# Performance work log

Measured on AMD Instinct MI355X. Metric: run time of the kernel, lower is better.

## Reference

```python
import jax, jax.numpy as jnp
import numpy as np

ALPHA = 0.2  # LeakyReLU negative slope
NEG_INF = -1e9


def setup_inputs() -> dict:
    key = jax.random.key(0)
    k1, k2, k3, k4 = jax.random.split(key, 4)
    B, N, Fin, Fout = 8, 2048, 128, 64
    h = jax.random.normal(k1, (B, N, Fin), dtype=jnp.float32)
    adj_mask = jax.random.randint(k2, (B, N, N), 0, 2).astype(jnp.int32)
    # xavier_uniform-style scales
    W = jax.random.uniform(k3, (Fout, Fin), dtype=jnp.float32,
                           minval=-1.0, maxval=1.0) * np.sqrt(6.0 / (Fin + Fout))
    a = jax.random.uniform(k4, (2 * Fout,), dtype=jnp.float32,
                           minval=-1.0, maxval=1.0) * np.sqrt(6.0 / (2 * Fout + 1))
    return {"h": h, "adj_mask": adj_mask, "W": W, "a": a}


def reference(h, adj_mask, W, a):
    # Wh: [B, N, Fout]
    Wh = jnp.einsum("bnf,of->bno", h, W)
    Fout = Wh.shape[-1]
    a1, a2 = a[:Fout], a[Fout:]
    # additive decomposition of a([Wh_i || Wh_j]): e_ij = leakyrelu(s1_i + s2_j)
    s1 = Wh @ a1  # [B, N]
    s2 = Wh @ a2  # [B, N]
    e = jax.nn.leaky_relu(s1[:, :, None] + s2[:, None, :], negative_slope=ALPHA)  # [B,N,N]
    e = jnp.where(adj_mask == 0, NEG_INF, e)
    attention = jax.nn.softmax(e, axis=-1)
    # dropout is identity in eval mode / p effectively 0 for the reference
    h_prime = jnp.einsum("bij,bjo->bio", attention, Wh)
    return h_prime
```

## Files before the change

kernel.cpp:

```cpp
#include <hip/hip_runtime.h>
#include <hip/hip_fp16.h>
#include <math.h>

#define LRELU_ALPHA 0.2f
#define NEG_INF -1000000000.0f
#define L2E 1.44269504088896340736f

constexpr int B_ = 8, N_ = 2048, FIN = 128, FOUT = 64;

typedef _Float16 __attribute__((ext_vector_type(8))) f16x8;
typedef float __attribute__((ext_vector_type(4))) f32x4;

__device__ __forceinline__ void gload16(const void* g, void* l) {
  __builtin_amdgcn_global_load_lds(
      (const __attribute__((address_space(1))) void*)g,
      (__attribute__((address_space(3))) void*)l, 16, 0, 0);
}

__global__ __launch_bounds__(256) void k_wh(
    const float* __restrict__ h, const float* __restrict__ W,
    const float* __restrict__ a, unsigned short* __restrict__ WhT,
    float* __restrict__ s1, float* __restrict__ s2) {
  __shared__ float Wt[128][65];
  __shared__ float hs[16][128];

  const int t = threadIdx.x;
  const int row0 = blockIdx.x * 16;

  for (int e = t; e < 64 * 128; e += 256) {
    int o = e >> 7, f = e & 127;
    Wt[f][o] = W[e];
  }
  {
    const float4* hg = (const float4*)(h + (size_t)row0 * FIN);
    for (int i4 = t; i4 < 16 * 32; i4 += 256) {
      int r = i4 >> 5, f4 = i4 & 31;
      *(float4*)&hs[r][f4 * 4] = hg[i4];
    }
  }
  __syncthreads();

  const int wave = t >> 6, lane = t & 63;
  float acc[4] = {0.f, 0.f, 0.f, 0.f};
#pragma unroll 4
  for (int f4 = 0; f4 < 32; ++f4) {
    float w0 = Wt[4 * f4 + 0][lane], w1 = Wt[4 * f4 + 1][lane];
    float w2 = Wt[4 * f4 + 2][lane], w3 = Wt[4 * f4 + 3][lane];
#pragma unroll
    for (int r = 0; r < 4; ++r) {
      float4 hv = *(const float4*)&hs[wave * 4 + r][f4 * 4];
      acc[r] += hv.x * w0 + hv.y * w1 + hv.z * w2 + hv.w * w3;
    }
  }

  const float a1v = a[lane], a2v = a[64 + lane];
  const int b = row0 / N_;
#pragma unroll
  for (int r = 0; r < 4; ++r) {
    const int row = row0 + wave * 4 + r;
    const int n = row - b * N_;
    const float v = acc[r];
    WhT[((size_t)b * 64 + lane) * N_ + n] = __half_as_ushort(__float2half(v));
    float p1 = v * a1v, p2 = v * a2v;
#pragma unroll
    for (int d = 32; d; d >>= 1) {
      p1 += __shfl_xor(p1, d, 64);
      p2 += __shfl_xor(p2, d, 64);
    }
    if (lane == 0) { s1[row] = p1; s2[row] = p2; }
  }
}

__global__ __launch_bounds__(256, 2) void k_attn(
    const unsigned short* __restrict__ WhT,
    const float* __restrict__ s1g, const float* __restrict__ s2g,
    const int* __restrict__ adj, float* __restrict__ out) {
  __shared__ __align__(16) unsigned char sbuf[4][8 * 1024];
  __shared__ float s2s[N_];

  const int t = threadIdx.x;
  const int wave = t >> 6, lane = t & 63;
  const int m = lane & 15, q = lane >> 4;
  const int b = blockIdx.y;
  const int i0 = blockIdx.x * 32;
  const int rg = wave & 1;
  const int p0 = (wave >> 1) * 2;

  const unsigned short* whB = WhT + (size_t)b * 64 * N_;
  const int* adjR = adj + (size_t)b * N_ * N_ + (size_t)(i0 + rg * 16 + m) * N_;

  {
    const float4* s2R = (const float4*)(s2g + (size_t)b * N_);
    for (int i = t; i < N_ / 4; i += 256) {
      float4 v = s2R[i];
      v.x *= L2E; v.y *= L2E; v.z *= L2E; v.w *= L2E;
      ((float4*)s2s)[i] = v;
    }
  }

  const float s1r = s1g[b * N_ + i0 + rg * 16 + m];
  const float c1 = (s1r - 2.0f) * L2E;
  const float c2 = (LRELU_ALPHA * s1r - 2.0f) * L2E;

  f16x8 ones;
#pragma unroll
  for (int j = 0; j < 8; ++j) ones[j] = (_Float16)1.0f;

  const unsigned char* whP0 =
      (const unsigned char*)(whB + (size_t)(wave * 16 + m) * N_ + q * 8);
  const unsigned char* whP1 = whP0 + 64;

#define STAGE(c)                                                            \
  {                                                                         \
    gload16(whP0 + (size_t)(c) * 128, &sbuf[(c) & 3][(wave * 2 + 0) * 1024]); \
    gload16(whP1 + (size_t)(c) * 128, &sbuf[(c) & 3][(wave * 2 + 1) * 1024]); \
  }
#define ISSUE_ADJ(S, c)                 \
  {                                     \
    const int* ap = adjR + (c) * 64 + q * 8; \
    S##0 = *(const int4*)(ap);          \
    S##1 = *(const int4*)(ap + 4);      \
    S##2 = *(const int4*)(ap + 32);     \
    S##3 = *(const int4*)(ap + 36);     \
  }
#define CONSUME(S, c)                                                        \
  {                                                                          \
    const unsigned char* Bb = &sbuf[(c) & 3][0];                             \
    _Pragma("unroll") for (int ks = 0; ks < 2; ++ks) {                       \
      int4 A0 = ks ? S##2 : S##0;                                            \
      int4 A1 = ks ? S##3 : S##1;                                            \
      const float* sp = &s2s[(c) * 64 + ks * 32 + q * 8];                    \
      float4 sv0 = *(const float4*)sp;                                       \
      float4 sv1 = *(const float4*)(sp + 4);                                 \
      float xs[8] = {sv0.x, sv0.y, sv0.z, sv0.w, sv1.x, sv1.y, sv1.z, sv1.w};\
      int avs[8] = {A0.x, A0.y, A0.z, A0.w, A1.x, A1.y, A1.z, A1.w};         \
      f16x8 af;                                                              \
      _Pragma("unroll") for (int j = 0; j < 8; ++j) {                        \
        float x = xs[j];                                                     \
        float e = fmaxf(c1 + x, fmaf(LRELU_ALPHA, x, c2));                   \
        e = avs[j] ? e : NEG_INF;                                            \
        af[j] = (_Float16)__builtin_amdgcn_exp2f(e);        \
      }                                                                      \
      f16x8 b0 = *(const f16x8*)(Bb + ((p0 + 0) * 2 + ks) * 1024 + lane * 16);\
      f16x8 b1 = *(const f16x8*)(Bb + ((p0 + 1) * 2 + ks) * 1024 + lane * 16);\
      acc0 = __builtin_amdgcn_mfma_f32_16x16x32_f16(af, b0, acc0, 0, 0, 0);  \
      acc1 = __builtin_amdgcn_mfma_f32_16x16x32_f16(af, b1, acc1, 0, 0, 0);  \
      accS = __builtin_amdgcn_mfma_f32_16x16x32_f16(af, ones, accS, 0, 0, 0);\
    }                                                                        \
  }
#define ITERX(c, S, VMS)                        \
  {                                             \
    asm volatile("s_waitcnt " VMS ::: "memory");\
    __builtin_amdgcn_s_barrier();               \
    CONSUME(S, c)                               \
  }

  int4 rA0, rA1, rA2, rA3, rB0, rB1, rB2, rB3, rC0, rC1, rC2, rC3;
  f32x4 acc0 = {0.f, 0.f, 0.f, 0.f}, acc1 = acc0, accS = acc0;

  ISSUE_ADJ(rA, 0) STAGE(0)
  ISSUE_ADJ(rB, 1) STAGE(1)
  ISSUE_ADJ(rC, 2) STAGE(2)
  __syncthreads();

  for (int cb = 0; cb < 27; cb += 3) {
    ITERX(cb + 0, rA, "vmcnt(12)") ISSUE_ADJ(rA, cb + 3) STAGE(cb + 3)
    ITERX(cb + 1, rB, "vmcnt(12)") ISSUE_ADJ(rB, cb + 4) STAGE(cb + 4)
    ITERX(cb + 2, rC, "vmcnt(12)") ISSUE_ADJ(rC, cb + 5) STAGE(cb + 5)
  }
  ITERX(27, rA, "vmcnt(12)") ISSUE_ADJ(rA, 30) STAGE(30)
  ITERX(28, rB, "vmcnt(12)") ISSUE_ADJ(rB, 31) STAGE(31)
  ITERX(29, rC, "vmcnt(12)")
  ITERX(30, rA, "vmcnt(6)")
  ITERX(31, rB, "vmcnt(0)")

#pragma unroll
  for (int r = 0; r < 4; ++r) {
    const int ri = q * 4 + r;
    const float l = accS[r];
    const float inv = (l == 0.f) ? 1.f : 1.f / l;
    const size_t row = (size_t)b * N_ + i0 + rg * 16 + ri;
    out[row * FOUT + (p0 + 0) * 16 + m] = acc0[r] * inv;
    out[row * FOUT + (p0 + 1) * 16 + m] = acc1[r] * inv;
  }
#undef STAGE
#undef ISSUE_ADJ
#undef CONSUME
#undef ITERX
}

extern "C" void kernel_launch(void* const* d_in, const int* in_sizes, int n_in,
                              void* d_out, int out_size, void* d_ws, size_t ws_size,
                              hipStream_t stream) {
  const float* h   = (const float*)d_in[0];
  const int*   adj = (const int*)d_in[1];
  const float* W   = (const float*)d_in[2];
  const float* a   = (const float*)d_in[3];
  float* out = (float*)d_out;

  unsigned short* WhT = (unsigned short*)d_ws;
  float* s1 = (float*)(WhT + (size_t)B_ * 64 * N_);
  float* s2 = s1 + (size_t)B_ * N_;

  k_wh<<<dim3(B_ * N_ / 16), 256, 0, stream>>>(h, W, a, WhT, s1, s2);
  k_attn<<<dim3(N_ / 32, B_), 256, 0, stream>>>(WhT, s1, s2, adj, out);
}
```

Before: 226.6 us.

## Bit-pack adjacency mask, split attention over key halves, add reduction kernel

A new pre-pass kernel reads the int32 adjacency mask once and packs it into 64-bit ballot words, laid out so each lane can pull its 8 mask bits per step. The attention kernel then reads the packed mask instead of int4 loads of int32 values. It loads WhT straight into registers rather than staging it through LDS with barriers, and splits the key dimension into two halves across a third grid axis, with a higher occupancy launch bound. Partial outputs and row sums go to workspace, and a small normalisation kernel combines them. This trades an extra full pass over the mask plus a partial-result round trip for a leaner, better-occupied main loop.

```diff
diff --git a/kernel.cpp b/kernel.cpp
--- a/kernel.cpp
+++ b/kernel.cpp
@@ -10,12 +10,6 @@
 
 typedef _Float16 __attribute__((ext_vector_type(8))) f16x8;
 typedef float __attribute__((ext_vector_type(4))) f32x4;
-
-__device__ __forceinline__ void gload16(const void* g, void* l) {
-  __builtin_amdgcn_global_load_lds(
-      (const __attribute__((address_space(1))) void*)g,
-      (__attribute__((address_space(3))) void*)l, 16, 0, 0);
-}
 
 __global__ __launch_bounds__(256) void k_wh(
     const float* __restrict__ h, const float* __restrict__ W,
@@ -71,122 +65,146 @@
   }
 }
 
-__global__ __launch_bounds__(256, 2) void k_attn(
+__global__ __launch_bounds__(256) void k_pack(
+    const int* __restrict__ adj, unsigned long long* __restrict__ pk) {
+  const int wave = threadIdx.x >> 6, lane = threadIdx.x & 63;
+  const size_t wid = (size_t)blockIdx.x * 4 + wave;
+  const int* src = adj + wid * 64 * 64 + lane;
+  unsigned long long* dst = pk + wid * 64;
+  for (int it = 0; it < 64; ++it) {
+    int v = src[it * 64];
+    unsigned long long mask = __ballot(v != 0);
+    unsigned long long o = 0;
+#pragma unroll
+    for (int qq = 0; qq < 4; ++qq) {
+      unsigned long long b0 = (mask >> (8 * qq)) & 0xFFull;
+      unsigned long long b1 = (mask >> (32 + 8 * qq)) & 0xFFull;
+      o |= (b0 | (b1 << 8)) << (16 * qq);
+    }
+    if (lane == 0) dst[it] = o;
+  }
+}
+
+__global__ __launch_bounds__(256, 4) void k_attn(
     const unsigned short* __restrict__ WhT,
     const float* __restrict__ s1g, const float* __restrict__ s2g,
-    const int* __restrict__ adj, float* __restrict__ out) {
-  __shared__ __align__(16) unsigned char sbuf[4][8 * 1024];
-  __shared__ float s2s[N_];
+    const unsigned short* __restrict__ pk,
+    float* __restrict__ pAcc, float* __restrict__ pSum) {
+  __shared__ float s2s[N_ / 2];
 
   const int t = threadIdx.x;
   const int wave = t >> 6, lane = t & 63;
   const int m = lane & 15, q = lane >> 4;
   const int b = blockIdx.y;
   const int i0 = blockIdx.x * 32;
+  const int js = blockIdx.z;
+  const int j0 = js * (N_ / 2);
   const int rg = wave & 1;
   const int p0 = (wave >> 1) * 2;
 
-  const unsigned short* whB = WhT + (size_t)b * 64 * N_;
-  const int* adjR = adj + (size_t)b * N_ * N_ + (size_t)(i0 + rg * 16 + m) * N_;
-
   {
-    const float4* s2R = (const float4*)(s2g + (size_t)b * N_);
-    for (int i = t; i < N_ / 4; i += 256) {
-      float4 v = s2R[i];
-      v.x *= L2E; v.y *= L2E; v.z *= L2E; v.w *= L2E;
-      ((float4*)s2s)[i] = v;
-    }
-  }
-
-  const float s1r = s1g[b * N_ + i0 + rg * 16 + m];
+    const float4* s2R = (const float4*)(s2g + (size_t)b * N_ + j0);
+    float4 v = s2R[t];
+    v.x *= L2E; v.y *= L2E; v.z *= L2E; v.w *= L2E;
+    ((float4*)s2s)[t] = v;
+  }
+
+  const int row_i = i0 + rg * 16 + m;
+  const float s1r = s1g[b * N_ + row_i];
   const float c1 = (s1r - 2.0f) * L2E;
   const float c2 = (LRELU_ALPHA * s1r - 2.0f) * L2E;
 
+  const unsigned short* whB = WhT + (size_t)b * 64 * N_;
+  const unsigned short* bp0 = whB + (size_t)(p0 * 16 + m) * N_ + j0 + q * 8;
+  const unsigned short* bp1 = whB + (size_t)((p0 + 1) * 16 + m) * N_ + j0 + q * 8;
+  const unsigned short* pkL =
+      pk + ((size_t)(b * N_ + row_i) * 32 + js * 16) * 4 + q;
+
   f16x8 ones;
 #pragma unroll
   for (int j = 0; j < 8; ++j) ones[j] = (_Float16)1.0f;
 
-  const unsigned char* whP0 =
-      (const unsigned char*)(whB + (size_t)(wave * 16 + m) * N_ + q * 8);
-  const unsigned char* whP1 = whP0 + 64;
-
-#define STAGE(c)                                                            \
-  {                                                                         \
-    gload16(whP0 + (size_t)(c) * 128, &sbuf[(c) & 3][(wave * 2 + 0) * 1024]); \
-    gload16(whP1 + (size_t)(c) * 128, &sbuf[(c) & 3][(wave * 2 + 1) * 1024]); \
-  }
-#define ISSUE_ADJ(S, c)                 \
-  {                                     \
-    const int* ap = adjR + (c) * 64 + q * 8; \
-    S##0 = *(const int4*)(ap);          \
-    S##1 = *(const int4*)(ap + 4);      \
-    S##2 = *(const int4*)(ap + 32);     \
-    S##3 = *(const int4*)(ap + 36);     \
-  }
-#define CONSUME(S, c)                                                        \
+  __syncthreads();
+
+  f32x4 acc0 = {0.f, 0.f, 0.f, 0.f}, acc1 = acc0, accS = acc0;
+
+  unsigned sA_w, sB_w;
+  f16x8 sA_b00, sA_b01, sA_b10, sA_b11;
+  f16x8 sB_b00, sB_b01, sB_b10, sB_b11;
+
+#define ISSUE(P, c)                                  \
+  {                                                  \
+    P##_w = (unsigned)pkL[(c) * 4];                  \
+    P##_b00 = *(const f16x8*)(bp0 + (c) * 64);       \
+    P##_b01 = *(const f16x8*)(bp0 + (c) * 64 + 32);  \
+    P##_b10 = *(const f16x8*)(bp1 + (c) * 64);       \
+    P##_b11 = *(const f16x8*)(bp1 + (c) * 64 + 32);  \
+  }
+#define CONSUME(P, c)                                                        \
   {                                                                          \
-    const unsigned char* Bb = &sbuf[(c) & 3][0];                             \
     _Pragma("unroll") for (int ks = 0; ks < 2; ++ks) {                       \
-      int4 A0 = ks ? S##2 : S##0;                                            \
-      int4 A1 = ks ? S##3 : S##1;                                            \
       const float* sp = &s2s[(c) * 64 + ks * 32 + q * 8];                    \
       float4 sv0 = *(const float4*)sp;                                       \
       float4 sv1 = *(const float4*)(sp + 4);                                 \
       float xs[8] = {sv0.x, sv0.y, sv0.z, sv0.w, sv1.x, sv1.y, sv1.z, sv1.w};\
-      int avs[8] = {A0.x, A0.y, A0.z, A0.w, A1.x, A1.y, A1.z, A1.w};         \
+      unsigned wb = P##_w >> (ks * 8);                                       \
       f16x8 af;                                                              \
       _Pragma("unroll") for (int j = 0; j < 8; ++j) {                        \
         float x = xs[j];                                                     \
         float e = fmaxf(c1 + x, fmaf(LRELU_ALPHA, x, c2));                   \
-        e = avs[j] ? e : NEG_INF;                                            \
+        e = ((wb >> j) & 1u) ? e : NEG_INF;                                  \
         af[j] = (_Float16)__builtin_amdgcn_exp2f(e);        \
       }                                                                      \
-      f16x8 b0 = *(const f16x8*)(Bb + ((p0 + 0) * 2 + ks) * 1024 + lane * 16);\
-      f16x8 b1 = *(const f16x8*)(Bb + ((p0 + 1) * 2 + ks) * 1024 + lane * 16);\
-      acc0 = __builtin_amdgcn_mfma_f32_16x16x32_f16(af, b0, acc0, 0, 0, 0);  \
-      acc1 = __builtin_amdgcn_mfma_f32_16x16x32_f16(af, b1, acc1, 0, 0, 0);  \
+      f16x8 B0 = ks ? P##_b01 : P##_b00;                                     \
+      f16x8 B1 = ks ? P##_b11 : P##_b10;                                     \
+      acc0 = __builtin_amdgcn_mfma_f32_16x16x32_f16(af, B0, acc0, 0, 0, 0);  \
+      acc1 = __builtin_amdgcn_mfma_f32_16x16x32_f16(af, B1, acc1, 0, 0, 0);  \
       accS = __builtin_amdgcn_mfma_f32_16x16x32_f16(af, ones, accS, 0, 0, 0);\
     }                                                                        \
   }
-#define ITERX(c, S, VMS)                        \
-  {                                             \
-    asm volatile("s_waitcnt " VMS ::: "memory");\
-    __builtin_amdgcn_s_barrier();               \
-    CONSUME(S, c)                               \
-  }
-
-  int4 rA0, rA1, rA2, rA3, rB0, rB1, rB2, rB3, rC0, rC1, rC2, rC3;
-  f32x4 acc0 = {0.f, 0.f, 0.f, 0.f}, acc1 = acc0, accS = acc0;
-
-  ISSUE_ADJ(rA, 0) STAGE(0)
-  ISSUE_ADJ(rB, 1) STAGE(1)
-  ISSUE_ADJ(rC, 2) STAGE(2)
-  __syncthreads();
-
-  for (int cb = 0; cb < 27; cb += 3) {
-    ITERX(cb + 0, rA, "vmcnt(12)") ISSUE_ADJ(rA, cb + 3) STAGE(cb + 3)
-    ITERX(cb + 1, rB, "vmcnt(12)") ISSUE_ADJ(rB, cb + 4) STAGE(cb + 4)
-    ITERX(cb + 2, rC, "vmcnt(12)") ISSUE_ADJ(rC, cb + 5) STAGE(cb + 5)
-  }
-  ITERX(27, rA, "vmcnt(12)") ISSUE_ADJ(rA, 30) STAGE(30)
-  ITERX(28, rB, "vmcnt(12)") ISSUE_ADJ(rB, 31) STAGE(31)
-  ITERX(29, rC, "vmcnt(12)")
-  ITERX(30, rA, "vmcnt(6)")
-  ITERX(31, rB, "vmcnt(0)")
+#define FENCE(VMS) asm volatile("s_waitcnt " VMS ::: "memory");
+
+  ISSUE(sA, 0)
+  ISSUE(sB, 1)
+  for (int c = 0; c < 14; c += 2) {
+    FENCE("vmcnt(5)")
+    CONSUME(sA, c) ISSUE(sA, c + 2)
+    FENCE("vmcnt(5)")
+    CONSUME(sB, c + 1) ISSUE(sB, c + 3)
+  }
+  FENCE("vmcnt(5)")
+  CONSUME(sA, 14)
+  FENCE("vmcnt(0)")
+  CONSUME(sB, 15)
 
 #pragma unroll
   for (int r = 0; r < 4; ++r) {
     const int ri = q * 4 + r;
-    const float l = accS[r];
-    const float inv = (l == 0.f) ? 1.f : 1.f / l;
-    const size_t row = (size_t)b * N_ + i0 + rg * 16 + ri;
-    out[row * FOUT + (p0 + 0) * 16 + m] = acc0[r] * inv;
-    out[row * FOUT + (p0 + 1) * 16 + m] = acc1[r] * inv;
-  }
-#undef STAGE
-#undef ISSUE_ADJ
+    const size_t row = (size_t)js * B_ * N_ + (size_t)b * N_ + i0 + rg * 16 + ri;
+    pAcc[row * FOUT + (p0 + 0) * 16 + m] = acc0[r];
+    pAcc[row * FOUT + (p0 + 1) * 16 + m] = acc1[r];
+    if (p0 == 0 && m == 0) pSum[row] = accS[r];
+  }
+#undef ISSUE
 #undef CONSUME
-#undef ITERX
+#undef FENCE
+}
+
+__global__ __launch_bounds__(256) void k_norm(
+    const float* __restrict__ pAcc, const float* __restrict__ pSum,
+    float* __restrict__ out) {
+  const int i4 = blockIdx.x * 256 + threadIdx.x;
+  const int row = i4 >> 4;
+  float4 v0 = ((const float4*)pAcc)[i4];
+  float4 v1 = ((const float4*)pAcc)[i4 + B_ * N_ * FOUT / 4];
+  const float l = pSum[row] + pSum[B_ * N_ + row];
+  const float inv = (l == 0.f) ? 1.f : 1.f / l;
+  float4 o;
+  o.x = (v0.x + v1.x) * inv;
+  o.y = (v0.y + v1.y) * inv;
+  o.z = (v0.z + v1.z) * inv;
+  o.w = (v0.w + v1.w) * inv;
+  ((float4*)out)[i4] = o;
 }
 
 extern "C" void kernel_launch(void* const* d_in, const int* in_sizes, int n_in,
@@ -201,7 +219,13 @@
   unsigned short* WhT = (unsigned short*)d_ws;
   float* s1 = (float*)(WhT + (size_t)B_ * 64 * N_);
   float* s2 = s1 + (size_t)B_ * N_;
-
+  float* pAcc = s2 + (size_t)B_ * N_;
+  float* pSum = pAcc + (size_t)2 * B_ * N_ * FOUT;
+  unsigned long long* pkw = (unsigned long long*)(pSum + (size_t)2 * B_ * N_);
+
+  k_pack<<<dim3(2048), 256, 0, stream>>>(adj, pkw);
   k_wh<<<dim3(B_ * N_ / 16), 256, 0, stream>>>(h, W, a, WhT, s1, s2);
-  k_attn<<<dim3(N_ / 32, B_), 256, 0, stream>>>(WhT, s1, s2, adj, out);
-}
+  k_attn<<<dim3(N_ / 32, B_, 2), 256, 0, stream>>>(
+      WhT, s1, s2, (const unsigned short*)pkw, pAcc, pSum);
+  k_norm<<<dim3(B_ * N_ * FOUT / 1024), 256, 0, stream>>>(pAcc, pSum, out);
+}
```

Result: slower. 272.3 us (+20.2%).

## Pre-pack adjacency mask into LDS bitmasks via ballot before attention loop

Applied to the files above, without the earlier changes.

The kernel no longer streams int32 adjacency values through registers inside the pipelined loop. Each block now reads its 32 rows of the mask up front with coalesced int4 loads, packs them into 64-bit ballot bitmasks in shared memory, and the main loop pulls mask bits from LDS. The loop becomes a 4-stage ring that only prefetches Wh tiles, with fewer outstanding vector loads and registers. The trade-off is a serialized prologue that reads all 256 KB of the block's mask before any compute can overlap it, plus extra bit-extraction ALU work in the inner loop.

```diff
diff --git a/kernel.cpp b/kernel.cpp
--- a/kernel.cpp
+++ b/kernel.cpp
@@ -76,6 +76,7 @@
     const float* __restrict__ s1g, const float* __restrict__ s2g,
     const int* __restrict__ adj, float* __restrict__ out) {
   __shared__ __align__(16) unsigned char sbuf[4][8 * 1024];
+  __shared__ unsigned long long pkls[32][34];
   __shared__ float s2s[N_];
 
   const int t = threadIdx.x;
@@ -86,8 +87,8 @@
   const int rg = wave & 1;
   const int p0 = (wave >> 1) * 2;
 
+  const int* adjB = adj + (size_t)b * N_ * N_;
   const unsigned short* whB = WhT + (size_t)b * 64 * N_;
-  const int* adjR = adj + (size_t)b * N_ * N_ + (size_t)(i0 + rg * 16 + m) * N_;
 
   {
     const float4* s2R = (const float4*)(s2g + (size_t)b * N_);
@@ -98,6 +99,26 @@
     }
   }
 
+  {
+    const int4* asrc = (const int4*)(adjB + (size_t)(i0 + wave * 8) * N_);
+    for (int r8 = 0; r8 < 8; ++r8) {
+      const int4* rs = asrc + (size_t)r8 * (N_ / 4);
+      unsigned long long* prow = &pkls[wave * 8 + r8][0];
+#pragma unroll
+      for (int k = 0; k < 8; ++k) {
+        int4 v = rs[k * 64 + lane];
+        unsigned long long b0 = __ballot(v.x != 0);
+        unsigned long long b1 = __ballot(v.y != 0);
+        unsigned long long b2 = __ballot(v.z != 0);
+        unsigned long long b3 = __ballot(v.w != 0);
+        unsigned long long sel = (lane == 0) ? b0
+                               : (lane == 1) ? b1
+                               : (lane == 2) ? b2 : b3;
+        if (lane < 4) prow[k * 4 + lane] = sel;
+      }
+    }
+  }
+
   const float s1r = s1g[b * N_ + i0 + rg * 16 + m];
   const float c1 = (s1r - 2.0f) * L2E;
   const float c2 = (LRELU_ALPHA * s1r - 2.0f) * L2E;
@@ -106,73 +127,74 @@
 #pragma unroll
   for (int j = 0; j < 8; ++j) ones[j] = (_Float16)1.0f;
 
-  const unsigned char* whP0 =
-      (const unsigned char*)(whB + (size_t)(wave * 16 + m) * N_ + q * 8);
-  const unsigned char* whP1 = whP0 + 64;
-
-#define STAGE(c)                                                            \
-  {                                                                         \
-    gload16(whP0 + (size_t)(c) * 128, &sbuf[(c) & 3][(wave * 2 + 0) * 1024]); \
-    gload16(whP1 + (size_t)(c) * 128, &sbuf[(c) & 3][(wave * 2 + 1) * 1024]); \
-  }
-#define ISSUE_ADJ(S, c)                 \
-  {                                     \
-    const int* ap = adjR + (c) * 64 + q * 8; \
-    S##0 = *(const int4*)(ap);          \
-    S##1 = *(const int4*)(ap + 4);      \
-    S##2 = *(const int4*)(ap + 32);     \
-    S##3 = *(const int4*)(ap + 36);     \
-  }
-#define CONSUME(S, c)                                                        \
+  const unsigned short* whP0 = whB + (size_t)(wave * 16 + m) * N_ + q * 8;
+  const unsigned short* whP1 = whP0 + 32;
+
+#define STAGE(S, c)                                           \
+  {                                                           \
+    gload16(whP0 + (c) * 64, (S) + (wave * 2 + 0) * 1024);    \
+    gload16(whP1 + (c) * 64, (S) + (wave * 2 + 1) * 1024);    \
+  }
+#define CONSUME(BASE, c)                                                     \
   {                                                                          \
-    const unsigned char* Bb = &sbuf[(c) & 3][0];                             \
     _Pragma("unroll") for (int ks = 0; ks < 2; ++ks) {                       \
-      int4 A0 = ks ? S##2 : S##0;                                            \
-      int4 A1 = ks ? S##3 : S##1;                                            \
+      const unsigned l0 =                                                    \
+          ((unsigned)((c)&3)) * 16u + (unsigned)ks * 8u + (unsigned)q * 2u;  \
+      const unsigned w0 = (unsigned)(mk01.x >> l0);                          \
+      const unsigned w1 = (unsigned)(mk01.y >> l0);                          \
+      const unsigned w2 = (unsigned)(mk23.x >> l0);                          \
+      const unsigned w3 = (unsigned)(mk23.y >> l0);                          \
       const float* sp = &s2s[(c) * 64 + ks * 32 + q * 8];                    \
       float4 sv0 = *(const float4*)sp;                                       \
       float4 sv1 = *(const float4*)(sp + 4);                                 \
       float xs[8] = {sv0.x, sv0.y, sv0.z, sv0.w, sv1.x, sv1.y, sv1.z, sv1.w};\
-      int avs[8] = {A0.x, A0.y, A0.z, A0.w, A1.x, A1.y, A1.z, A1.w};         \
       f16x8 af;                                                              \
       _Pragma("unroll") for (int j = 0; j < 8; ++j) {                        \
         float x = xs[j];                                                     \
         float e = fmaxf(c1 + x, fmaf(LRELU_ALPHA, x, c2));                   \
-        e = avs[j] ? e : NEG_INF;                                            \
+        const unsigned sel = ((j & 3) == 0) ? w0                             \
+                           : ((j & 3) == 1) ? w1                             \
+                           : ((j & 3) == 2) ? w2 : w3;                       \
+        e = ((sel >> (j >> 2)) & 1u) ? e : NEG_INF;                          \
         af[j] = (_Float16)__builtin_amdgcn_exp2f(e);        \
       }                                                                      \
-      f16x8 b0 = *(const f16x8*)(Bb + ((p0 + 0) * 2 + ks) * 1024 + lane * 16);\
-      f16x8 b1 = *(const f16x8*)(Bb + ((p0 + 1) * 2 + ks) * 1024 + lane * 16);\
+      f16x8 b0 =                                                             \
+          *(const f16x8*)((BASE) + ((p0 + 0) * 2 + ks) * 1024 + lane * 16);  \
+      f16x8 b1 =                                                             \
+          *(const f16x8*)((BASE) + ((p0 + 1) * 2 + ks) * 1024 + lane * 16);  \
       acc0 = __builtin_amdgcn_mfma_f32_16x16x32_f16(af, b0, acc0, 0, 0, 0);  \
       acc1 = __builtin_amdgcn_mfma_f32_16x16x32_f16(af, b1, acc1, 0, 0, 0);  \
       accS = __builtin_amdgcn_mfma_f32_16x16x32_f16(af, ones, accS, 0, 0, 0);\
     }                                                                        \
   }
-#define ITERX(c, S, VMS)                        \
-  {                                             \
-    asm volatile("s_waitcnt " VMS ::: "memory");\
-    __builtin_amdgcn_s_barrier();               \
-    CONSUME(S, c)                               \
-  }
-
-  int4 rA0, rA1, rA2, rA3, rB0, rB1, rB2, rB3, rC0, rC1, rC2, rC3;
+#define FV(NN) asm volatile("s_waitcnt vmcnt(" #NN ")" ::: "memory");
+#define BAR() __builtin_amdgcn_s_barrier();
+
   f32x4 acc0 = {0.f, 0.f, 0.f, 0.f}, acc1 = acc0, accS = acc0;
-
-  ISSUE_ADJ(rA, 0) STAGE(0)
-  ISSUE_ADJ(rB, 1) STAGE(1)
-  ISSUE_ADJ(rC, 2) STAGE(2)
+  const unsigned long long* mrow = &pkls[rg * 16 + m][0];
+
+  STAGE(sbuf[0], 0)
+  STAGE(sbuf[1], 1)
+  STAGE(sbuf[2], 2)
   __syncthreads();
 
-  for (int cb = 0; cb < 27; cb += 3) {
-    ITERX(cb + 0, rA, "vmcnt(12)") ISSUE_ADJ(rA, cb + 3) STAGE(cb + 3)
-    ITERX(cb + 1, rB, "vmcnt(12)") ISSUE_ADJ(rB, cb + 4) STAGE(cb + 4)
-    ITERX(cb + 2, rC, "vmcnt(12)") ISSUE_ADJ(rC, cb + 5) STAGE(cb + 5)
-  }
-  ITERX(27, rA, "vmcnt(12)") ISSUE_ADJ(rA, 30) STAGE(30)
-  ITERX(28, rB, "vmcnt(12)") ISSUE_ADJ(rB, 31) STAGE(31)
-  ITERX(29, rC, "vmcnt(12)")
-  ITERX(30, rA, "vmcnt(6)")
-  ITERX(31, rB, "vmcnt(0)")
+  for (int g = 0; g < 7; ++g) {
+    ulonglong2 mk01 = *(const ulonglong2*)(mrow + g * 4);
+    ulonglong2 mk23 = *(const ulonglong2*)(mrow + g * 4 + 2);
+    const int c = 4 * g;
+    FV(4) BAR() CONSUME(sbuf[0], c + 0) STAGE(sbuf[3], c + 3)
+    FV(4) BAR() CONSUME(sbuf[1], c + 1) STAGE(sbuf[0], c + 4)
+    FV(4) BAR() CONSUME(sbuf[2], c + 2) STAGE(sbuf[1], c + 5)
+    FV(4) BAR() CONSUME(sbuf[3], c + 3) STAGE(sbuf[2], c + 6)
+  }
+  {
+    ulonglong2 mk01 = *(const ulonglong2*)(mrow + 28);
+    ulonglong2 mk23 = *(const ulonglong2*)(mrow + 30);
+    FV(4) BAR() CONSUME(sbuf[0], 28) STAGE(sbuf[3], 31)
+    FV(4) BAR() CONSUME(sbuf[1], 29)
+    FV(2) BAR() CONSUME(sbuf[2], 30)
+    FV(0) BAR() CONSUME(sbuf[3], 31)
+  }
 
 #pragma unroll
   for (int r = 0; r < 4; ++r) {
@@ -184,9 +206,9 @@
     out[row * FOUT + (p0 + 1) * 16 + m] = acc1[r] * inv;
   }
 #undef STAGE
-#undef ISSUE_ADJ
 #undef CONSUME
-#undef ITERX
+#undef FV
+#undef BAR
 }
 
 extern "C" void kernel_launch(void* const* d_in, const int* in_sizes, int n_in,
```

Result: slower. 249.4 us (+10.1%).
